# Kernel tuning notes

Measured on AMD Instinct MI355X. Metric: run time of the kernel, lower is better.

## Reference

```python
import jax, jax.numpy as jnp
import numpy as np

OBS_DIM = 1024
HEADS = 16
SCALE = OBS_DIM ** (-0.5)  # note: full obs_dim, as in the original module


def setup_inputs() -> dict:
    key = jax.random.key(0)
    k1, k2, k3, k4 = jax.random.split(key, 4)
    x = jax.random.normal(k1, (4, 2048, OBS_DIM), dtype=jnp.float32)
    # torch nn.Linear weight layout: [out_features, in_features]
    w_qkv = jax.random.normal(k2, (3 * OBS_DIM, OBS_DIM), dtype=jnp.float32) * (OBS_DIM ** -0.5)
    w_out = jax.random.normal(k3, (OBS_DIM, OBS_DIM), dtype=jnp.float32) * (OBS_DIM ** -0.5)
    b_out = jax.random.normal(k4, (OBS_DIM,), dtype=jnp.float32) * 0.02
    return {"x": x, "w_qkv": w_qkv, "w_out": w_out, "b_out": b_out}


def reference(x, w_qkv, w_out, b_out):
    b, n, dm = x.shape
    h = HEADS
    d = dm // h
    qkv = x @ w_qkv.T  # [b, n, 3*dm]
    # rearrange 'b n (c h d) -> c b h n d'
    qkv = qkv.reshape(b, n, 3, h, d)
    q = jnp.transpose(qkv[:, :, 0], (0, 2, 1, 3))  # [b,h,n,d]
    k = jnp.transpose(qkv[:, :, 1], (0, 2, 1, 3))
    v = jnp.transpose(qkv[:, :, 2], (0, 2, 1, 3))
    scores = jnp.einsum('bhid,bhjd->bhij', q, k) * SCALE
    att = jax.nn.softmax(scores, axis=-1)
    ctx = jnp.einsum('bhij,bhjd->bhid', att, v)  # [b,h,n,d]
    ctx = jnp.transpose(ctx, (0, 2, 1, 3)).reshape(b, n, dm)
    return ctx @ w_out.T + b_out
```

## Files before the change

kernel.cpp:

```cpp
#include <hip/hip_runtime.h>
#include <hip/hip_bf16.h>


typedef __attribute__((ext_vector_type(8))) short short8;
typedef __attribute__((ext_vector_type(4))) float float4x;

#define QS 8388608

#if __has_builtin(__builtin_amdgcn_exp2f)
#define FASTEXP(x) __builtin_amdgcn_exp2f(x)
#define QPRESCALE 0.0450842203f
#else
#define FASTEXP(x) __expf(x)
#define QPRESCALE 0.03125f
#endif

static __device__ __forceinline__ short f2bf(float f) {
    union { float f; unsigned u; } x; x.f = f;
    unsigned r = x.u + 0x7fffu + ((x.u >> 16) & 1u);
    return (short)(r >> 16);
}
static __device__ __forceinline__ unsigned pack2(float a, float b) {
    return (unsigned)(unsigned short)f2bf(a) | ((unsigned)(unsigned short)f2bf(b) << 16);
}
static __device__ __forceinline__ unsigned fbits(float f) {
    union { float f; unsigned u; } x; x.f = f; return x.u;
}
static __device__ __forceinline__ unsigned permpack(float lo, float hi) {
    return __builtin_amdgcn_perm(fbits(hi), fbits(lo), 0x07060302u);
}
static __device__ __forceinline__ void async16(const void* g, void* l) {
    __builtin_amdgcn_global_load_lds(
        (const __attribute__((address_space(1))) void*)g,
        (__attribute__((address_space(3))) void*)l, 16, 0, 0);
}

__global__ __launch_bounds__(256) void cast_kernel(
    const float* __restrict__ x, const float* __restrict__ wq, const float* __restrict__ wo,
    short* __restrict__ xo, short* __restrict__ wqo, short* __restrict__ woo)
{
    int i = blockIdx.x * 256 + threadIdx.x;
    const float* src; short* dst; int off;
    if (i < 2097152)      { src = x;  dst = xo;  off = i; }
    else if (i < 2883584) { src = wq; dst = wqo; off = i - 2097152; }
    else                  { src = wo; dst = woo; off = i - 2883584; }
    float4 v = *(const float4*)(src + (size_t)off * 4);
    unsigned t[2] = {pack2(v.x, v.y), pack2(v.z, v.w)};
    *(uint2*)(dst + (size_t)off * 4) = *(uint2*)t;
}

template<int MODE>
__global__ __launch_bounds__(256) void gemm_bt_kernel(
    const short* __restrict__ A, const short* __restrict__ W,
    const float* __restrict__ bias, void* __restrict__ outp,
    int M, int N, int K)
{
    __shared__ short sh[32768];
    short* const A0 = sh;
    short* const W0 = sh + 8192;
    short* const A1 = sh + 16384;
    short* const W1 = sh + 24576;

    const int tid  = threadIdx.x;
    const int lane = tid & 63;
    const int wave = tid >> 6;
    const int row16 = lane & 15;
    const int quad  = lane >> 4;
    const int wm = wave >> 1, wn = wave & 1;

    const int l  = blockIdx.y * 64 + blockIdx.x;
    const int xcd = l & 7, s = l >> 3;
    const int m0 = (xcd * 8 + (s & 7)) * 128;
    const int n0 = (s >> 3) * 128;

    float4x acc[4][4] = {};

    auto stageAW = [&](int kb, short* Ad, short* Wd) {
        for (int r = 0; r < 4; r++) {
            int i = r * 256 + tid, row = i >> 3, cc = i & 7, sc = cc ^ (row & 7);
            async16(A + (size_t)(m0 + row) * K + kb + sc * 8, Ad + i * 8);
        }
        for (int r = 0; r < 4; r++) {
            int i = r * 256 + tid, row = i >> 3, cc = i & 7, sc = cc ^ (row & 7);
            async16(W + (size_t)(n0 + row) * K + kb + sc * 8, Wd + i * 8);
        }
    };

    stageAW(0, A0, W0);
    __syncthreads();
    const int KI = K >> 6;
    for (int ki = 0; ki < KI; ki++) {
        short* const Ac = (ki & 1) ? A1 : A0;
        short* const Wc = (ki & 1) ? W1 : W0;
        short* const An = (ki & 1) ? A0 : A1;
        short* const Wn = (ki & 1) ? W0 : W1;
        if (ki + 1 < KI) stageAW((ki + 1) << 6, An, Wn);

        short8 af[4][2], bfr[4][2];
        for (int mt = 0; mt < 4; mt++)
            for (int h = 0; h < 2; h++) {
                int row = wm * 64 + mt * 16 + row16;
                af[mt][h] = *(const short8*)&Ac[row * 64 + (((h << 2) | quad) ^ (row & 7)) * 8];
            }
        for (int nt = 0; nt < 4; nt++)
            for (int h = 0; h < 2; h++) {
                int row = wn * 64 + nt * 16 + row16;
                bfr[nt][h] = *(const short8*)&Wc[row * 64 + (((h << 2) | quad) ^ (row & 7)) * 8];
            }
        for (int mt = 0; mt < 4; mt++)
            for (int nt = 0; nt < 4; nt++) {
                acc[mt][nt] = __builtin_amdgcn_mfma_f32_16x16x32_bf16(af[mt][0], bfr[nt][0], acc[mt][nt], 0, 0, 0);
                acc[mt][nt] = __builtin_amdgcn_mfma_f32_16x16x32_bf16(af[mt][1], bfr[nt][1], acc[mt][nt], 0, 0, 0);
            }
        __syncthreads();
    }

    if (MODE == 0) {
        for (int mt = 0; mt < 4; mt++)
            for (int nt = 0; nt < 4; nt++)
                for (int r = 0; r < 4; r++) {
                    int mm = m0 + wm * 64 + mt * 16 + quad * 4 + r;
                    int nn = n0 + wn * 64 + nt * 16 + row16;
                    ((float*)outp)[(size_t)mm * N + nn] = acc[mt][nt][r] + bias[nn];
                }
    } else {
        const int c  = n0 >> 10;
        const int bb = m0 >> 11;
        for (int nt = 0; nt < 4; nt++) {
            const int rem = (n0 & 1023) + wn * 64 + nt * 16 + row16;
            const int hh = rem >> 6, dd = rem & 63;
            for (int mt = 0; mt < 4; mt++) {
                const int nsq0 = (m0 & 2047) + wm * 64 + mt * 16 + quad * 4;
                if (c == 2) {
                    size_t off = 2 * (size_t)QS + (((size_t)(bb * 16 + hh) * 64 + dd) * 2048 + nsq0);
                    uint2 w;
                    w.x = pack2(acc[mt][nt][0], acc[mt][nt][1]);
                    w.y = pack2(acc[mt][nt][2], acc[mt][nt][3]);
                    *(uint2*)((short*)outp + off) = w;
                } else {
                    size_t off = (size_t)c * QS + (((size_t)(bb * 16 + hh) * 2048 + nsq0) * 64 + dd);
                    const float scl = (c == 0) ? QPRESCALE : 1.f;
                    for (int r = 0; r < 4; r++)
                        ((short*)outp)[off + (size_t)r * 64] = f2bf(acc[mt][nt][r] * scl);
                }
            }
        }
    }
}

static __device__ __forceinline__ void stage_kv(
    const short* __restrict__ Km, const short* __restrict__ VT,
    size_t basekq, size_t basev, int kt, short* k_dst, short* v_dst, int tid)
{
    for (int r = 0; r < 2; r++) {
        int i = r * 256 + tid, row = i >> 3, cc = i & 7, sc = cc ^ (row & 7);
        async16(Km + basekq + (size_t)(kt * 64 + row) * 64 + sc * 8, k_dst + i * 8);
    }
    for (int r = 0; r < 2; r++) {
        int i = r * 256 + tid, row = i >> 3, cc = i & 7, sc = cc ^ (row & 7);
        async16(VT + basev + (size_t)row * 2048 + kt * 64 + sc * 8, v_dst + i * 8);
    }
}

__global__ __launch_bounds__(256) void flash_kernel(
    const short* __restrict__ Q, const short* __restrict__ Km,
    const short* __restrict__ VT, short* __restrict__ ctx)
{
    __shared__ __align__(16) short sh[20480];

    const int id   = blockIdx.y * 16 + blockIdx.x;
    const int slot = id >> 3;
    const int bh   = (id & 7) * 8 + (slot & 7);
    const int qt   = slot >> 3;

    const int tid  = threadIdx.x;
    const int wave = tid >> 6;
    const int lane = tid & 63;
    const int row16 = lane & 15;
    const int quad  = lane >> 4;
    const size_t basekq = (size_t)bh * 2048 * 64;
    const size_t basev  = (size_t)bh * 64 * 2048;

    short* const bufA = sh;
    short* const bufB = sh + 8192;
    short* const Psw  = sh + 16384 + wave * 1024;

    for (int r = 0; r < 4; r++) {
        int i = r * 256 + tid, row = i >> 3, cc = i & 7, sc = cc ^ (row & 7);
        async16(Q + basekq + (size_t)(qt * 128 + row) * 64 + sc * 8, &bufA[i * 8]);
    }
    stage_kv(Km, VT, basekq, basev, 0, bufB, bufB + 4096, tid);
    __syncthreads();
    short8 q[2][2];
    for (int u = 0; u < 2; u++)
        for (int h = 0; h < 2; h++) {
            int row = wave * 32 + u * 16 + row16;
            q[u][h] = *(const short8*)&bufA[row * 64 + (((h << 2) | quad) ^ (row & 7)) * 8];
        }
    __syncthreads();

    short8 ones8;
    for (int e = 0; e < 8; e++) ones8[e] = (short)0x3F80;

    float4x accO[2][4] = {};
    float4x accL[2] = {};

    const int pw0 = row16 * 64;
    const int psl[4] = {
        ((0 * 2 + (quad >> 1)) ^ (row16 & 7)) * 8 + (quad & 1) * 4,
        ((1 * 2 + (quad >> 1)) ^ (row16 & 7)) * 8 + (quad & 1) * 4,
        ((2 * 2 + (quad >> 1)) ^ (row16 & 7)) * 8 + (quad & 1) * 4,
        ((3 * 2 + (quad >> 1)) ^ (row16 & 7)) * 8 + (quad & 1) * 4};
    const int prd0 = (quad ^ (row16 & 7)) * 8;
    const int prd1 = ((4 + quad) ^ (row16 & 7)) * 8;

    for (int kt = 0; kt < 32; kt++) {
        short* const cur = (kt & 1) ? bufA : bufB;
        short* const nxt = (kt & 1) ? bufB : bufA;
        if (kt < 31)
            stage_kv(Km, VT, basekq, basev, kt + 1, nxt, nxt + 4096, tid);

        short8 kf[4][2], vf[4][2];
        for (int jt = 0; jt < 4; jt++)
            for (int h = 0; h < 2; h++) {
                int row = jt * 16 + row16;
                int sl = (((h << 2) | quad) ^ (row & 7)) * 8;
                kf[jt][h] = *(const short8*)&cur[row * 64 + sl];
                vf[jt][h] = *(const short8*)&cur[4096 + row * 64 + sl];
            }

        for (int u = 0; u < 2; u++) {
            float4x sf[4];
            for (int jt = 0; jt < 4; jt++) {
                float4x s0 = {};
                s0 = __builtin_amdgcn_mfma_f32_16x16x32_bf16(kf[jt][0], q[u][0], s0, 0, 0, 0);
                s0 = __builtin_amdgcn_mfma_f32_16x16x32_bf16(kf[jt][1], q[u][1], s0, 0, 0, 0);
                sf[jt] = s0;
            }
            __builtin_amdgcn_wave_barrier();
            for (int jt = 0; jt < 4; jt++) {
                float e0 = FASTEXP(sf[jt][0]), e1 = FASTEXP(sf[jt][1]);
                float e2 = FASTEXP(sf[jt][2]), e3 = FASTEXP(sf[jt][3]);
                uint2 w; w.x = permpack(e0, e1); w.y = permpack(e2, e3);
                *(uint2*)&Psw[pw0 + psl[jt]] = w;
            }
            __builtin_amdgcn_wave_barrier();
            short8 p0 = *(const short8*)&Psw[pw0 + prd0];
            short8 p1 = *(const short8*)&Psw[pw0 + prd1];
            for (int dt = 0; dt < 4; dt++) {
                accO[u][dt] = __builtin_amdgcn_mfma_f32_16x16x32_bf16(vf[dt][0], p0, accO[u][dt], 0, 0, 0);
                accO[u][dt] = __builtin_amdgcn_mfma_f32_16x16x32_bf16(vf[dt][1], p1, accO[u][dt], 0, 0, 0);
            }
            accL[u] = __builtin_amdgcn_mfma_f32_16x16x32_bf16(ones8, p0, accL[u], 0, 0, 0);
            accL[u] = __builtin_amdgcn_mfma_f32_16x16x32_bf16(ones8, p1, accL[u], 0, 0, 0);
        }
        __syncthreads();
    }
    const int bb = bh >> 4, hh = bh & 15;
    for (int u = 0; u < 2; u++) {
        const float inv = 1.f / accL[u][0];
        const int nrow = qt * 128 + wave * 32 + u * 16 + row16;
        for (int dt = 0; dt < 4; dt++) {
            uint2 w;
            w.x = pack2(accO[u][dt][0] * inv, accO[u][dt][1] * inv);
            w.y = pack2(accO[u][dt][2] * inv, accO[u][dt][3] * inv);
            *(uint2*)(ctx + (size_t)(bb * 2048 + nrow) * 1024 + hh * 64 + dt * 16 + quad * 4) = w;
        }
    }
}

extern "C" void kernel_launch(void* const* d_in, const int* in_sizes, int n_in,
                              void* d_out, int out_size, void* d_ws, size_t ws_size,
                              hipStream_t stream) {
    const float* x     = (const float*)d_in[0];
    const float* w_qkv = (const float*)d_in[1];
    const float* w_out = (const float*)d_in[2];
    const float* b_out = (const float*)d_in[3];
    float* out = (float*)d_out;
    short* ws  = (short*)d_ws;

    short* qkv_ws  = ws;
    short* xbf     = ws + (size_t)3 * QS;
    short* ctx_ws  = xbf;
    short* wqkv_bf = ws + (size_t)4 * QS;
    short* wout_bf = wqkv_bf + 3145728;

    dim3 blk(256);
    cast_kernel<<<12288, blk, 0, stream>>>(x, w_qkv, w_out, xbf, wqkv_bf, wout_bf);
    gemm_bt_kernel<1><<<dim3(64, 24), blk, 0, stream>>>(xbf, wqkv_bf, nullptr, qkv_ws,
                                                        8192, 3072, 1024);
    flash_kernel<<<dim3(16, 64), blk, 0, stream>>>(qkv_ws, qkv_ws + QS, qkv_ws + 2 * (size_t)QS,
                                                   ctx_ws);
    gemm_bt_kernel<0><<<dim3(64, 8), blk, 0, stream>>>(ctx_ws, wout_bf, b_out, out,
                                                       8192, 1024, 1024);
}
```

Before: 259.0 us.

## Feed P directly from registers into 16x16x16 MFMA, dropping LDS round-trip

The exp'd score fragments now go straight from the QK^T MFMA output layout into 16x16x16 bf16 MFMAs as the B operand. This removes the per-wave P scratchpad in LDS, its writes and reads, and the wave barriers around them. V is read from LDS in a matching 4-element layout. The cost is twice as many (smaller-K) MFMA instructions for PV and the row sum. Shared memory shrinks and launch bounds request 4 blocks per CU, which may raise occupancy but also limits registers.

```diff
diff --git a/kernel.cpp b/kernel.cpp
--- a/kernel.cpp
+++ b/kernel.cpp
@@ -3,6 +3,7 @@
 
 
 typedef __attribute__((ext_vector_type(8))) short short8;
+typedef __attribute__((ext_vector_type(4))) short bf16x4;
 typedef __attribute__((ext_vector_type(4))) float float4x;
 
 #define QS 8388608
@@ -13,6 +14,21 @@
 #else
 #define FASTEXP(x) __expf(x)
 #define QPRESCALE 0.03125f
+#endif
+
+#if __has_builtin(__builtin_amdgcn_mfma_f32_16x16x16bf16_1k)
+static __device__ __forceinline__ float4x mfma16(bf16x4 a, bf16x4 b, float4x c) {
+    return __builtin_amdgcn_mfma_f32_16x16x16bf16_1k(a, b, c, 0, 0, 0);
+}
+#elif __has_builtin(__builtin_amdgcn_mfma_f32_16x16x16_bf16)
+static __device__ __forceinline__ float4x mfma16(bf16x4 a, bf16x4 b, float4x c) {
+    return __builtin_amdgcn_mfma_f32_16x16x16_bf16(a, b, c, 0, 0, 0);
+}
+#else
+static __device__ __forceinline__ float4x mfma16(bf16x4 a, bf16x4 b, float4x c) {
+    asm("v_mfma_f32_16x16x16_bf16 %0, %1, %2, %0" : "+v"(c) : "v"(a), "v"(b));
+    return c;
+}
 #endif
 
 static __device__ __forceinline__ short f2bf(float f) {
@@ -162,11 +178,11 @@
     }
 }
 
-__global__ __launch_bounds__(256) void flash_kernel(
+__global__ __launch_bounds__(256, 4) void flash_kernel(
     const short* __restrict__ Q, const short* __restrict__ Km,
     const short* __restrict__ VT, short* __restrict__ ctx)
 {
-    __shared__ __align__(16) short sh[20480];
+    __shared__ __align__(16) short sh[16384];
 
     const int id   = blockIdx.y * 16 + blockIdx.x;
     const int slot = id >> 3;
@@ -183,7 +199,6 @@
 
     short* const bufA = sh;
     short* const bufB = sh + 8192;
-    short* const Psw  = sh + 16384 + wave * 1024;
 
     for (int r = 0; r < 4; r++) {
         int i = r * 256 + tid, row = i >> 3, cc = i & 7, sc = cc ^ (row & 7);
@@ -199,20 +214,11 @@
         }
     __syncthreads();
 
-    short8 ones8;
-    for (int e = 0; e < 8; e++) ones8[e] = (short)0x3F80;
+    bf16x4 ones4;
+    for (int e = 0; e < 4; e++) ones4[e] = (short)0x3F80;
 
     float4x accO[2][4] = {};
     float4x accL[2] = {};
-
-    const int pw0 = row16 * 64;
-    const int psl[4] = {
-        ((0 * 2 + (quad >> 1)) ^ (row16 & 7)) * 8 + (quad & 1) * 4,
-        ((1 * 2 + (quad >> 1)) ^ (row16 & 7)) * 8 + (quad & 1) * 4,
-        ((2 * 2 + (quad >> 1)) ^ (row16 & 7)) * 8 + (quad & 1) * 4,
-        ((3 * 2 + (quad >> 1)) ^ (row16 & 7)) * 8 + (quad & 1) * 4};
-    const int prd0 = (quad ^ (row16 & 7)) * 8;
-    const int prd1 = ((4 + quad) ^ (row16 & 7)) * 8;
 
     for (int kt = 0; kt < 32; kt++) {
         short* const cur = (kt & 1) ? bufA : bufB;
@@ -220,13 +226,18 @@
         if (kt < 31)
             stage_kv(Km, VT, basekq, basev, kt + 1, nxt, nxt + 4096, tid);
 
-        short8 kf[4][2], vf[4][2];
+        short8 kf[4][2];
         for (int jt = 0; jt < 4; jt++)
             for (int h = 0; h < 2; h++) {
                 int row = jt * 16 + row16;
-                int sl = (((h << 2) | quad) ^ (row & 7)) * 8;
-                kf[jt][h] = *(const short8*)&cur[row * 64 + sl];
-                vf[jt][h] = *(const short8*)&cur[4096 + row * 64 + sl];
+                kf[jt][h] = *(const short8*)&cur[row * 64 + ((((h << 2) | quad) ^ (row & 7))) * 8];
+            }
+        bf16x4 va[4][4];
+        for (int dt = 0; dt < 4; dt++)
+            for (int jt = 0; jt < 4; jt++) {
+                int row = dt * 16 + row16;
+                va[dt][jt] = *(const bf16x4*)&cur[4096 + row * 64
+                              + (((2 * jt + (quad >> 1)) ^ (row & 7))) * 8 + (quad & 1) * 4];
             }
 
         for (int u = 0; u < 2; u++) {
@@ -237,22 +248,20 @@
                 s0 = __builtin_amdgcn_mfma_f32_16x16x32_bf16(kf[jt][1], q[u][1], s0, 0, 0, 0);
                 sf[jt] = s0;
             }
-            __builtin_amdgcn_wave_barrier();
+            bf16x4 pb[4];
             for (int jt = 0; jt < 4; jt++) {
                 float e0 = FASTEXP(sf[jt][0]), e1 = FASTEXP(sf[jt][1]);
                 float e2 = FASTEXP(sf[jt][2]), e3 = FASTEXP(sf[jt][3]);
-                uint2 w; w.x = permpack(e0, e1); w.y = permpack(e2, e3);
-                *(uint2*)&Psw[pw0 + psl[jt]] = w;
-            }
-            __builtin_amdgcn_wave_barrier();
-            short8 p0 = *(const short8*)&Psw[pw0 + prd0];
-            short8 p1 = *(const short8*)&Psw[pw0 + prd1];
-            for (int dt = 0; dt < 4; dt++) {
-                accO[u][dt] = __builtin_amdgcn_mfma_f32_16x16x32_bf16(vf[dt][0], p0, accO[u][dt], 0, 0, 0);
-                accO[u][dt] = __builtin_amdgcn_mfma_f32_16x16x32_bf16(vf[dt][1], p1, accO[u][dt], 0, 0, 0);
-            }
-            accL[u] = __builtin_amdgcn_mfma_f32_16x16x32_bf16(ones8, p0, accL[u], 0, 0, 0);
-            accL[u] = __builtin_amdgcn_mfma_f32_16x16x32_bf16(ones8, p1, accL[u], 0, 0, 0);
+                union { uint2 u2; bf16x4 s; } pk;
+                pk.u2.x = permpack(e0, e1);
+                pk.u2.y = permpack(e2, e3);
+                pb[jt] = pk.s;
+            }
+            for (int jt = 0; jt < 4; jt++)
+                accL[u] = mfma16(ones4, pb[jt], accL[u]);
+            for (int dt = 0; dt < 4; dt++)
+                for (int jt = 0; jt < 4; jt++)
+                    accO[u][dt] = mfma16(va[dt][jt], pb[jt], accO[u][dt]);
         }
         __syncthreads();
     }
```

Measured after the change: 248.2 us. -4.2%, faster.

## Enlarge flash query tile, shuffle P via permlane swaps, sum rows in registers

Applied to the files above, without the earlier changes.

The flash kernel now handles 256 query rows per block (64 per wave) instead of 128, so each staged K/V tile is reused across twice as many queries and the grid halves. The P-matrix round trip through LDS is replaced by permlane32/permlane16 register swaps that rebuild the MFMA B operand directly. The row-sum MFMAs against a ones vector are replaced by scalar accumulation plus cross-lane shuffles at the end. Q is loaded straight from global into registers. The costs are higher register pressure (launch bounds now ask for 2 blocks) and fewer blocks to fill the GPU.

```diff
diff --git a/kernel.cpp b/kernel.cpp
--- a/kernel.cpp
+++ b/kernel.cpp
@@ -4,6 +4,7 @@
 
 typedef __attribute__((ext_vector_type(8))) short short8;
 typedef __attribute__((ext_vector_type(4))) float float4x;
+typedef __attribute__((ext_vector_type(2))) unsigned uint2x;
 
 #define QS 8388608
 
@@ -14,6 +15,27 @@
 #define FASTEXP(x) __expf(x)
 #define QPRESCALE 0.03125f
 #endif
+
+static __device__ __forceinline__ float4x mfma32(short8 a, short8 b, float4x c) {
+    return __builtin_amdgcn_mfma_f32_16x16x32_bf16(a, b, c, 0, 0, 0);
+}
+
+static __device__ __forceinline__ void pl32swap(unsigned &a, unsigned &b) {
+#if __has_builtin(__builtin_amdgcn_permlane32_swap)
+    uint2x r = __builtin_amdgcn_permlane32_swap(a, b, false, false);
+    a = r[0]; b = r[1];
+#else
+    asm("v_permlane32_swap_b32 %0, %1" : "+v"(a), "+v"(b));
+#endif
+}
+static __device__ __forceinline__ void pl16swap(unsigned &a, unsigned &b) {
+#if __has_builtin(__builtin_amdgcn_permlane16_swap)
+    uint2x r = __builtin_amdgcn_permlane16_swap(a, b, false, false);
+    a = r[0]; b = r[1];
+#else
+    asm("v_permlane16_swap_b32 %0, %1" : "+v"(a), "+v"(b));
+#endif
+}
 
 static __device__ __forceinline__ short f2bf(float f) {
     union { float f; unsigned u; } x; x.f = f;
@@ -162,16 +184,15 @@
     }
 }
 
-__global__ __launch_bounds__(256) void flash_kernel(
+__global__ __launch_bounds__(256, 2) void flash_kernel(
     const short* __restrict__ Q, const short* __restrict__ Km,
     const short* __restrict__ VT, short* __restrict__ ctx)
 {
-    __shared__ __align__(16) short sh[20480];
-
-    const int id   = blockIdx.y * 16 + blockIdx.x;
-    const int slot = id >> 3;
-    const int bh   = (id & 7) * 8 + (slot & 7);
-    const int qt   = slot >> 3;
+    __shared__ __align__(16) short sh[16384];
+
+    const int id = blockIdx.y * 8 + blockIdx.x;
+    const int bh = ((id & 7) << 3) | ((id >> 3) & 7);
+    const int qt = id >> 6;
 
     const int tid  = threadIdx.x;
     const int wave = tid >> 6;
@@ -183,36 +204,20 @@
 
     short* const bufA = sh;
     short* const bufB = sh + 8192;
-    short* const Psw  = sh + 16384 + wave * 1024;
-
-    for (int r = 0; r < 4; r++) {
-        int i = r * 256 + tid, row = i >> 3, cc = i & 7, sc = cc ^ (row & 7);
-        async16(Q + basekq + (size_t)(qt * 128 + row) * 64 + sc * 8, &bufA[i * 8]);
+
+    short8 q[4][2];
+    {
+        const int qrow0 = qt * 256 + wave * 64 + row16;
+        for (int u = 0; u < 4; u++)
+            for (int h = 0; h < 2; h++)
+                q[u][h] = *(const short8*)(Q + basekq
+                            + (size_t)(qrow0 + u * 16) * 64 + (size_t)(((h << 2) | quad)) * 8);
     }
     stage_kv(Km, VT, basekq, basev, 0, bufB, bufB + 4096, tid);
     __syncthreads();
-    short8 q[2][2];
-    for (int u = 0; u < 2; u++)
-        for (int h = 0; h < 2; h++) {
-            int row = wave * 32 + u * 16 + row16;
-            q[u][h] = *(const short8*)&bufA[row * 64 + (((h << 2) | quad) ^ (row & 7)) * 8];
-        }
-    __syncthreads();
-
-    short8 ones8;
-    for (int e = 0; e < 8; e++) ones8[e] = (short)0x3F80;
-
-    float4x accO[2][4] = {};
-    float4x accL[2] = {};
-
-    const int pw0 = row16 * 64;
-    const int psl[4] = {
-        ((0 * 2 + (quad >> 1)) ^ (row16 & 7)) * 8 + (quad & 1) * 4,
-        ((1 * 2 + (quad >> 1)) ^ (row16 & 7)) * 8 + (quad & 1) * 4,
-        ((2 * 2 + (quad >> 1)) ^ (row16 & 7)) * 8 + (quad & 1) * 4,
-        ((3 * 2 + (quad >> 1)) ^ (row16 & 7)) * 8 + (quad & 1) * 4};
-    const int prd0 = (quad ^ (row16 & 7)) * 8;
-    const int prd1 = ((4 + quad) ^ (row16 & 7)) * 8;
+
+    float4x accO[4][4] = {};
+    float lsum[4] = {0.f, 0.f, 0.f, 0.f};
 
     for (int kt = 0; kt < 32; kt++) {
         short* const cur = (kt & 1) ? bufA : bufB;
@@ -224,42 +229,52 @@
         for (int jt = 0; jt < 4; jt++)
             for (int h = 0; h < 2; h++) {
                 int row = jt * 16 + row16;
-                int sl = (((h << 2) | quad) ^ (row & 7)) * 8;
+                int sl = ((((h << 2) | quad) ^ (row & 7))) * 8;
                 kf[jt][h] = *(const short8*)&cur[row * 64 + sl];
                 vf[jt][h] = *(const short8*)&cur[4096 + row * 64 + sl];
             }
 
-        for (int u = 0; u < 2; u++) {
+        for (int u = 0; u < 4; u++) {
             float4x sf[4];
             for (int jt = 0; jt < 4; jt++) {
                 float4x s0 = {};
-                s0 = __builtin_amdgcn_mfma_f32_16x16x32_bf16(kf[jt][0], q[u][0], s0, 0, 0, 0);
-                s0 = __builtin_amdgcn_mfma_f32_16x16x32_bf16(kf[jt][1], q[u][1], s0, 0, 0, 0);
+                s0 = mfma32(kf[jt][0], q[u][0], s0);
+                s0 = mfma32(kf[jt][1], q[u][1], s0);
                 sf[jt] = s0;
             }
-            __builtin_amdgcn_wave_barrier();
+            unsigned wA[4][2];
             for (int jt = 0; jt < 4; jt++) {
                 float e0 = FASTEXP(sf[jt][0]), e1 = FASTEXP(sf[jt][1]);
                 float e2 = FASTEXP(sf[jt][2]), e3 = FASTEXP(sf[jt][3]);
-                uint2 w; w.x = permpack(e0, e1); w.y = permpack(e2, e3);
-                *(uint2*)&Psw[pw0 + psl[jt]] = w;
-            }
-            __builtin_amdgcn_wave_barrier();
-            short8 p0 = *(const short8*)&Psw[pw0 + prd0];
-            short8 p1 = *(const short8*)&Psw[pw0 + prd1];
+                lsum[u] += (e0 + e1) + (e2 + e3);
+                wA[jt][0] = permpack(e0, e1);
+                wA[jt][1] = permpack(e2, e3);
+            }
+            short8 pf[2];
+            for (int jp = 0; jp < 2; jp++) {
+                unsigned a0 = wA[jp * 2][0], b0 = wA[jp * 2 + 1][0];
+                unsigned a1 = wA[jp * 2][1], b1 = wA[jp * 2 + 1][1];
+                pl32swap(a0, b0); pl16swap(a0, b0);
+                pl32swap(a1, b1); pl16swap(a1, b1);
+                union { unsigned w[4]; short8 s; } pk;
+                pk.w[0] = a0; pk.w[1] = a1; pk.w[2] = b0; pk.w[3] = b1;
+                pf[jp] = pk.s;
+            }
             for (int dt = 0; dt < 4; dt++) {
-                accO[u][dt] = __builtin_amdgcn_mfma_f32_16x16x32_bf16(vf[dt][0], p0, accO[u][dt], 0, 0, 0);
-                accO[u][dt] = __builtin_amdgcn_mfma_f32_16x16x32_bf16(vf[dt][1], p1, accO[u][dt], 0, 0, 0);
-            }
-            accL[u] = __builtin_amdgcn_mfma_f32_16x16x32_bf16(ones8, p0, accL[u], 0, 0, 0);
-            accL[u] = __builtin_amdgcn_mfma_f32_16x16x32_bf16(ones8, p1, accL[u], 0, 0, 0);
+                accO[u][dt] = mfma32(vf[dt][0], pf[0], accO[u][dt]);
+                accO[u][dt] = mfma32(vf[dt][1], pf[1], accO[u][dt]);
+            }
         }
         __syncthreads();
     }
+
     const int bb = bh >> 4, hh = bh & 15;
-    for (int u = 0; u < 2; u++) {
-        const float inv = 1.f / accL[u][0];
-        const int nrow = qt * 128 + wave * 32 + u * 16 + row16;
+    for (int u = 0; u < 4; u++) {
+        float l = lsum[u];
+        l += __shfl_xor(l, 16);
+        l += __shfl_xor(l, 32);
+        const float inv = 1.f / l;
+        const int nrow = qt * 256 + wave * 64 + u * 16 + row16;
         for (int dt = 0; dt < 4; dt++) {
             uint2 w;
             w.x = pack2(accO[u][dt][0] * inv, accO[u][dt][1] * inv);
@@ -289,8 +304,8 @@
     cast_kernel<<<12288, blk, 0, stream>>>(x, w_qkv, w_out, xbf, wqkv_bf, wout_bf);
     gemm_bt_kernel<1><<<dim3(64, 24), blk, 0, stream>>>(xbf, wqkv_bf, nullptr, qkv_ws,
                                                         8192, 3072, 1024);
-    flash_kernel<<<dim3(16, 64), blk, 0, stream>>>(qkv_ws, qkv_ws + QS, qkv_ws + 2 * (size_t)QS,
-                                                   ctx_ws);
+    flash_kernel<<<dim3(8, 64), blk, 0, stream>>>(qkv_ws, qkv_ws + QS, qkv_ws + 2 * (size_t)QS,
+                                                  ctx_ws);
     gemm_bt_kernel<0><<<dim3(64, 8), blk, 0, stream>>>(ctx_ws, wout_bf, b_out, out,
                                                        8192, 1024, 1024);
 }
```

Result: faster. 239.8 us (-7.4%).
